# Optimization experiments

Measured on AMD Instinct MI355X. Metric: run time of the kernel, lower is better.

The kernel has to match this reference:

```python
import jax, jax.numpy as jnp
import numpy as np

B, T, C = 4, 2048, 1024
HEADS = 16
HEAD_DIM = C // HEADS
WINDOW = 256


def setup_inputs() -> dict:
    key = jax.random.key(0)
    k1, k2, k3 = jax.random.split(key, 3)
    x = jax.random.normal(k1, (B, T, C), dtype=jnp.float32)
    # torch nn.Linear weights: [out_features, in_features]; scale like kaiming-uniform-ish
    W_qkv = jax.random.normal(k2, (3 * C, C), dtype=jnp.float32) * (1.0 / np.sqrt(C))
    W_proj = jax.random.normal(k3, (C, C), dtype=jnp.float32) * (1.0 / np.sqrt(C))
    return {"x": x, "W_qkv": W_qkv, "W_proj": W_proj}


def reference(x, W_qkv, W_proj):
    b, t, c = x.shape
    h, d = HEADS, HEAD_DIM
    qkv = x @ W_qkv.T  # [b,t,3c]
    q, k, v = jnp.split(qkv, 3, axis=-1)
    q = q.reshape(b, t, h, d).transpose(0, 2, 1, 3)  # [b,h,t,d]
    k = k.reshape(b, t, h, d).transpose(0, 2, 1, 3)
    v = v.reshape(b, t, h, d).transpose(0, 2, 1, 3)
    scale = 1.0 / jnp.sqrt(jnp.asarray(d, dtype=q.dtype))
    scores = jnp.einsum('bhqd,bhkd->bhqk', q, k) * scale  # [b,h,t,t]
    i = jnp.arange(t)[:, None]
    j = jnp.arange(t)[None, :]
    mask = (j <= i) & (j > i - WINDOW)  # sliding-window causal band
    scores = jnp.where(mask, scores, -jnp.inf)
    attn = jax.nn.softmax(scores, axis=-1)
    y = jnp.einsum('bhqk,bhkd->bhqd', attn, v)  # [b,h,t,d]
    y = y.transpose(0, 2, 1, 3).reshape(b, t, c)
    return y @ W_proj.T
```

## Files before the change

### kernel.cpp

```cpp
#include <hip/hip_runtime.h>
#include <hip/hip_bf16.h>
#include <math.h>

#define BB 4
#define TT 2048
#define CC 1024
#define HH 16
#define DD 64
#define WW 256
#define MM (BB*TT)
#define NX (MM*CC)
#define NQ (3*CC*CC)
#define NP (CC*CC)

typedef __bf16 bf16x8 __attribute__((ext_vector_type(8)));
typedef __bf16 bf16x4 __attribute__((ext_vector_type(4)));
typedef float  f32x4  __attribute__((ext_vector_type(4)));

__device__ __forceinline__ void async_cp16(const void* g, void* l) {
  __builtin_amdgcn_global_load_lds(
      (const __attribute__((address_space(1))) void*)g,
      (__attribute__((address_space(3))) void*)l, 16, 0, 0);
}

__device__ __forceinline__ unsigned short f2bf(float v) {
  __hip_bfloat16 h = __float2bfloat16(v);
  return *(unsigned short*)&h;
}

__device__ __forceinline__ size_t wpk_off(int n, int k) {
  return ((((size_t)(n >> 7) * 16 + (k >> 6)) * 16) +
          (((k >> 3) & 7) * 2 + ((n >> 6) & 1))) * 512 +
         (size_t)(n & 63) * 8 + (k & 7);
}

__global__ __launch_bounds__(256)
void prep(const float* __restrict__ x,
          const float* __restrict__ wq,
          const float* __restrict__ wp,
          unsigned short* __restrict__ wpk,
          unsigned short* __restrict__ Apk) {
  const int p = blockIdx.x;
  const int tid = threadIdx.x;
  if (p < 4096) {
    int i = (p * 256 + tid) * 4;
    const float* src; unsigned short* dst; int n, k;
    if (i < NQ) { src = wq + i; n = i >> 10; k = i & 1023; dst = wpk; }
    else {
      int j = i - NQ;
      src = wp + j; n = j >> 10; k = j & 1023; dst = wpk + NQ;
    }
    float4 v = *(const float4*)src;
    size_t off = wpk_off(n, k);
    dst[off + 0] = f2bf(v.x);
    dst[off + 1] = f2bf(v.y);
    dst[off + 2] = f2bf(v.z);
    dst[off + 3] = f2bf(v.w);
    return;
  }
  __shared__ __align__(16) unsigned short tile[64 * 72];
  const int pid = p - 4096;
  const int bm = pid & 127;
  const int bk = pid >> 7;
  const int tr = tid >> 4;
  const int tc = (tid & 15) * 4;
#pragma unroll
  for (int i = 0; i < 4; i++) {
    int row = i * 16 + tr;
    float4 v = *(const float4*)&x[(size_t)(bm * 64 + row) * 1024 + bk * 64 + tc];
    tile[row * 72 + tc + 0] = f2bf(v.x);
    tile[row * 72 + tc + 1] = f2bf(v.y);
    tile[row * 72 + tc + 2] = f2bf(v.z);
    tile[row * 72 + tc + 3] = f2bf(v.w);
  }
  __syncthreads();
  const int w = tid >> 6, lane = tid & 63;
  const int quad = lane >> 4, l15 = lane & 15;
#pragma unroll
  for (int f = 0; f < 2; f++) {
    bf16x8 fr = *(const bf16x8*)&tile[(w * 16 + l15) * 72 + f * 32 + quad * 8];
    *(bf16x8*)&Apk[(((size_t)(bm * 4 + w) * 32) + bk * 2 + f) * 512 + lane * 8] = fr;
  }
}

__global__ __launch_bounds__(256, 2)
void gemm_qkv(const unsigned short* __restrict__ Apk,
              const unsigned short* __restrict__ Bw,
              unsigned short* __restrict__ Qh,
              unsigned short* __restrict__ Kh,
              unsigned short* __restrict__ Vt) {
  __shared__ __align__(16) unsigned short Bs[4][8192];

  const int id   = blockIdx.x;
  const int xcd  = id & 7;
  const int slot = id >> 3;
  const int mloc = slot / 24;
  const int nloc = slot % 24;
  const int m0 = (xcd * 4 + mloc) * 256;
  const int n0 = nloc * 128;

  const int tid  = threadIdx.x;
  const int w    = tid >> 6;
  const int lane = tid & 63;
  const int quad = lane >> 4;
  const int l15  = lane & 15;

  f32x4 acc[4][8];
#pragma unroll
  for (int i = 0; i < 4; i++)
#pragma unroll
    for (int j = 0; j < 8; j++) acc[i][j] = (f32x4)0.0f;

  const unsigned short* abase =
      Apk + ((size_t)((m0 >> 4) + w * 4) * 32) * 512 + lane * 8;

  const unsigned short* wb = Bw + (size_t)(n0 >> 7) * (16 * 16 * 512);

  auto stageB = [&](int kt, unsigned short* bs) {
#pragma unroll
    for (int i = 0; i < 4; i++) {
      int idx = w + 4 * i;
      async_cp16(wb + ((size_t)kt * 16 + idx) * 512 + lane * 8,
                 &bs[idx * 512]);
    }
  };

  bf16x8 Af[3][4];
  auto loadA = [&](int g, bf16x8* fr) {
#pragma unroll
    for (int tm = 0; tm < 4; tm++)
      fr[tm] = *(const bf16x8*)(abase + ((size_t)(tm * 32 + g)) * 512);
  };

  loadA(0, Af[0]);
  loadA(1, Af[1]);
  stageB(0, Bs[0]);
  stageB(1, Bs[1]);
  stageB(2, Bs[2]);
  asm volatile("s_waitcnt vmcnt(0)" ::: "memory");
  __builtin_amdgcn_sched_barrier(0);
  asm volatile("s_barrier" ::: "memory");

#pragma unroll
  for (int s = 0; s < 16; s++) {
    const unsigned short* bs = Bs[s & 3];
    if (s + 3 < 16) stageB(s + 3, Bs[(s + 3) & 3]);
#pragma unroll
    for (int sub = 0; sub < 2; sub++) {
      const int g = s * 2 + sub;
      if (g + 2 < 32) loadA(g + 2, Af[(g + 2) % 3]);
      const bf16x8* af = Af[g % 3];
      __builtin_amdgcn_s_setprio(1);
#pragma unroll
      for (int tn = 0; tn < 8; tn++) {
        bf16x8 bfv = *(const bf16x8*)
            &bs[(sub * 4 + quad) * 1024 + (tn * 16 + l15) * 8];
#pragma unroll
        for (int tm = 0; tm < 4; tm++)
          acc[tm][tn] = __builtin_amdgcn_mfma_f32_16x16x32_bf16(
              af[tm], bfv, acc[tm][tn], 0, 0, 0);
      }
      __builtin_amdgcn_s_setprio(0);
    }
    asm volatile("s_waitcnt vmcnt(16) lgkmcnt(0)" ::: "memory");
    __builtin_amdgcn_sched_barrier(0);
    asm volatile("s_barrier" ::: "memory");
  }

  const int t3 = n0 >> 10;
  if (t3 == 0) {
#pragma unroll
    for (int tm = 0; tm < 4; tm++)
#pragma unroll
      for (int tn = 0; tn < 8; tn++) {
        int colb = n0 + tn * 16;
        int hh = (colb >> 6) & 15;
        int dd = (colb & 63) + l15;
#pragma unroll
        for (int r = 0; r < 4; r++) {
          int row = m0 + w * 64 + tm * 16 + quad * 4 + r;
          int b = row >> 11, tt = row & 2047;
          Qh[((size_t)((b * 16 + hh) * 2048 + tt)) * 64 + dd] =
              f2bf(acc[tm][tn][r] * 0.125f);
        }
      }
  } else if (t3 == 1) {
#pragma unroll
    for (int tm = 0; tm < 4; tm++)
#pragma unroll
      for (int tn = 0; tn < 8; tn++) {
        int colb = n0 + tn * 16;
        int hh = (colb >> 6) & 15;
        int dd = (colb & 63) + l15;
#pragma unroll
        for (int r = 0; r < 4; r++) {
          int row = m0 + w * 64 + tm * 16 + quad * 4 + r;
          int b = row >> 11, tt = row & 2047;
          Kh[((((size_t)(b * 16 + hh) * 32 + (tt >> 6)) * 8 + (dd >> 3)) * 512)
             + (tt & 63) * 8 + (dd & 7)] = f2bf(acc[tm][tn][r]);
        }
      }
  } else {
    unsigned short* T = &Bs[0][0] + w * 4608;
    const int b    = (m0 + w * 64) >> 11;
    const int tc_g = ((m0 & 2047) >> 6) + w;
    const int h0   = (n0 >> 6) & 15;
#pragma unroll
    for (int hp = 0; hp < 2; hp++) {
#pragma unroll
      for (int tnl = 0; tnl < 4; tnl++)
#pragma unroll
        for (int tm = 0; tm < 4; tm++)
#pragma unroll
          for (int r = 0; r < 4; r++)
            T[(tnl * 16 + l15) * 72 + tm * 16 + quad * 4 + r] =
                f2bf(acc[tm][hp * 4 + tnl][r]);
      asm volatile("s_waitcnt lgkmcnt(0)" ::: "memory");
      const size_t base =
          ((size_t)((b * 16 + h0 + hp) * 32 + tc_g)) * 4096;
#pragma unroll
      for (int j = 0; j < 8; j++) {
        bf16x8 v = *(const bf16x8*)&T[lane * 72 + j * 8];
        *(bf16x8*)&Vt[base + (size_t)j * 512 + lane * 8] = v;
      }
    }
  }
}

__global__ __launch_bounds__(256, 2)
void gemm_proj(const unsigned short* __restrict__ Apk,
               const unsigned short* __restrict__ Bw,
               float* __restrict__ Co) {
  __shared__ __align__(16) unsigned short Bs[4][8192];

  const int id   = blockIdx.x;
  const int xcd  = id & 7;
  const int slot = id >> 3;
  const int mloc = slot >> 3;
  const int nloc = slot & 7;
  const int m0 = (xcd * 8 + mloc) * 128;
  const int n0 = nloc * 128;

  const int tid  = threadIdx.x;
  const int w    = tid >> 6;
  const int lane = tid & 63;
  const int quad = lane >> 4;
  const int l15  = lane & 15;

  f32x4 acc[2][8];
#pragma unroll
  for (int i = 0; i < 2; i++)
#pragma unroll
    for (int j = 0; j < 8; j++) acc[i][j] = (f32x4)0.0f;

  const unsigned short* abase =
      Apk + ((size_t)((m0 >> 4) + w * 2) * 32) * 512 + lane * 8;

  const unsigned short* wb = Bw + (size_t)(n0 >> 7) * (16 * 16 * 512);

  auto stageB = [&](int kt, unsigned short* bs) {
#pragma unroll
    for (int i = 0; i < 4; i++) {
      int idx = w + 4 * i;
      async_cp16(wb + ((size_t)kt * 16 + idx) * 512 + lane * 8,
                 &bs[idx * 512]);
    }
  };

  bf16x8 Af[3][2];
  auto loadA = [&](int g, bf16x8* fr) {
#pragma unroll
    for (int tm = 0; tm < 2; tm++)
      fr[tm] = *(const bf16x8*)(abase + ((size_t)(tm * 32 + g)) * 512);
  };

  loadA(0, Af[0]);
  loadA(1, Af[1]);
  stageB(0, Bs[0]);
  stageB(1, Bs[1]);
  stageB(2, Bs[2]);
  asm volatile("s_waitcnt vmcnt(0)" ::: "memory");
  __builtin_amdgcn_sched_barrier(0);
  asm volatile("s_barrier" ::: "memory");

#pragma unroll
  for (int s = 0; s < 16; s++) {
    const unsigned short* bs = Bs[s & 3];
    if (s + 3 < 16) stageB(s + 3, Bs[(s + 3) & 3]);
#pragma unroll
    for (int sub = 0; sub < 2; sub++) {
      const int g = s * 2 + sub;
      if (g + 2 < 32) loadA(g + 2, Af[(g + 2) % 3]);
      const bf16x8* af = Af[g % 3];
      __builtin_amdgcn_s_setprio(1);
#pragma unroll
      for (int tn = 0; tn < 8; tn++) {
        bf16x8 bfv = *(const bf16x8*)
            &bs[(sub * 4 + quad) * 1024 + (tn * 16 + l15) * 8];
#pragma unroll
        for (int tm = 0; tm < 2; tm++)
          acc[tm][tn] = __builtin_amdgcn_mfma_f32_16x16x32_bf16(
              af[tm], bfv, acc[tm][tn], 0, 0, 0);
      }
      __builtin_amdgcn_s_setprio(0);
    }
    if (s < 14)
      asm volatile("s_waitcnt vmcnt(12) lgkmcnt(0)" ::: "memory");
    else
      asm volatile("s_waitcnt vmcnt(8) lgkmcnt(0)" ::: "memory");
    __builtin_amdgcn_sched_barrier(0);
    asm volatile("s_barrier" ::: "memory");
  }

#pragma unroll
  for (int tm = 0; tm < 2; tm++)
#pragma unroll
    for (int tn = 0; tn < 8; tn++)
#pragma unroll
      for (int r = 0; r < 4; r++) {
        int row = m0 + w * 32 + tm * 16 + quad * 4 + r;
        int col = n0 + tn * 16 + l15;
        Co[(size_t)row * 1024 + col] = acc[tm][tn][r];
      }
}

__global__ __launch_bounds__(256, 2)
void attn_mfma(const unsigned short* __restrict__ Qh,
               const unsigned short* __restrict__ Kh,
               const unsigned short* __restrict__ Vt,
               unsigned short* __restrict__ Ypk) {
  __shared__ __align__(16) unsigned short SH[40960];

  const int tid  = threadIdx.x;
  const int w    = tid >> 6;
  const int lane = tid & 63;
  const int quad = lane >> 4;
  const int l15  = lane & 15;

  const int vid  = blockIdx.y * 32 + blockIdx.x;
  const int v    = (vid & 7) * 256 + (vid >> 3);
  const int bh   = v >> 5;
  const int q0   = (v & 31) << 6;

  const int c0 = (q0 >= 256) ? 0 : (4 - (q0 >> 6));

  const unsigned short* Qg = Qh + ((size_t)bh * 2048 + q0) * 64;
  bf16x8 Qf[2];
#pragma unroll
  for (int fs = 0; fs < 2; fs++)
    Qf[fs] = *(const bf16x8*)(Qg + (w * 16 + l15) * 64 + fs * 32 + quad * 8);

  const unsigned short* Kg = Kh + (size_t)bh * 32 * 4096;
  const unsigned short* Vg = Vt + (size_t)bh * 32 * 4096;
  for (int ch = c0; ch < 5; ch++) {
    int tc = (q0 >> 6) - 4 + ch;
#pragma unroll
    for (int i = 0; i < 2; i++) {
      int kc = w * 2 + i;
      async_cp16(Kg + ((size_t)tc * 8 + kc) * 512 + lane * 8,
                 &SH[ch * 4096 + kc * 512]);
    }
  }
  for (int ch = c0; ch < 5; ch++) {
    int tc = (q0 >> 6) - 4 + ch;
#pragma unroll
    for (int i = 0; i < 2; i++) {
      int kc = w * 2 + i;
      async_cp16(Vg + ((size_t)tc * 8 + kc) * 512 + lane * 8,
                 &SH[20480 + ch * 4096 + kc * 512]);
    }
  }
  if (c0 == 0)      asm volatile("s_waitcnt vmcnt(10)" ::: "memory");
  else if (c0 == 1) asm volatile("s_waitcnt vmcnt(8)"  ::: "memory");
  else if (c0 == 2) asm volatile("s_waitcnt vmcnt(6)"  ::: "memory");
  else if (c0 == 3) asm volatile("s_waitcnt vmcnt(4)"  ::: "memory");
  else              asm volatile("s_waitcnt vmcnt(2)"  ::: "memory");
  __builtin_amdgcn_sched_barrier(0);
  asm volatile("s_barrier" ::: "memory");

  f32x4 S[5][4];
#pragma unroll
  for (int ch = 0; ch < 5; ch++)
#pragma unroll
    for (int tn = 0; tn < 4; tn++) S[ch][tn] = (f32x4)0.0f;

#pragma unroll
  for (int ch = 0; ch < 5; ch++) {
    if (ch < c0) continue;
#pragma unroll
    for (int ks = 0; ks < 2; ks++) {
      int kc = ks * 4 + quad;
#pragma unroll
      for (int tn = 0; tn < 4; tn++) {
        bf16x8 bk = *(const bf16x8*)
            &SH[ch * 4096 + kc * 512 + (tn * 16 + l15) * 8];
        S[ch][tn] = __builtin_amdgcn_mfma_f32_16x16x32_bf16(
            Qf[ks], bk, S[ch][tn], 0, 0, 0);
      }
    }
  }

  const int qb = q0 + w * 16 + quad * 4;
  if (c0 == 0) {
#pragma unroll
    for (int tn = 0; tn < 4; tn++) {
      int j = q0 - 256 + tn * 16 + l15;
#pragma unroll
      for (int r = 0; r < 4; r++)
        if (qb + r > j + (WW - 1)) S[0][tn][r] = -__builtin_inff();
    }
  }
#pragma unroll
  for (int tn = 0; tn < 4; tn++) {
    int j = q0 + tn * 16 + l15;
#pragma unroll
    for (int r = 0; r < 4; r++)
      if (j > qb + r) S[4][tn][r] = -__builtin_inff();
  }

  float mrow[4], lrow[4];
#pragma unroll
  for (int r = 0; r < 4; r++) mrow[r] = -__builtin_inff();
#pragma unroll
  for (int ch = 0; ch < 5; ch++) {
    if (ch < c0) continue;
#pragma unroll
    for (int tn = 0; tn < 4; tn++)
#pragma unroll
      for (int r = 0; r < 4; r++)
        mrow[r] = fmaxf(mrow[r], S[ch][tn][r]);
  }
#pragma unroll
  for (int off = 1; off < 16; off <<= 1)
#pragma unroll
    for (int r = 0; r < 4; r++)
      mrow[r] = fmaxf(mrow[r], __shfl_xor(mrow[r], off));

#pragma unroll
  for (int r = 0; r < 4; r++) lrow[r] = 0.0f;
#pragma unroll
  for (int ch = 0; ch < 5; ch++) {
    if (ch < c0) continue;
#pragma unroll
    for (int tn = 0; tn < 4; tn++)
#pragma unroll
      for (int r = 0; r < 4; r++) {
        float e = __expf(S[ch][tn][r] - mrow[r]);
        S[ch][tn][r] = e;
        lrow[r] += e;
      }
  }
#pragma unroll
  for (int off = 1; off < 16; off <<= 1)
#pragma unroll
    for (int r = 0; r < 4; r++) lrow[r] += __shfl_xor(lrow[r], off);

  asm volatile("s_waitcnt vmcnt(0)" ::: "memory");
  __builtin_amdgcn_sched_barrier(0);
  asm volatile("s_barrier" ::: "memory");

  f32x4 Oacc[4];
#pragma unroll
  for (int td = 0; td < 4; td++) Oacc[td] = (f32x4)0.0f;

#pragma unroll
  for (int ch = 0; ch < 5; ch++) {
    if (ch < c0) continue;
    unsigned short* Ps = SH + (ch & 1) * 4608;
#pragma unroll
    for (int tn = 0; tn < 4; tn++)
#pragma unroll
      for (int r = 0; r < 4; r++)
        Ps[(w * 16 + quad * 4 + r) * 68 + tn * 16 + l15] = f2bf(S[ch][tn][r]);
    asm volatile("s_waitcnt lgkmcnt(0)" ::: "memory");
#pragma unroll
    for (int ks = 0; ks < 2; ks++) {
      int off = (w * 16 + l15) * 68 + ks * 32 + quad * 8;
      bf16x4 plo = *(const bf16x4*)&Ps[off];
      bf16x4 phi = *(const bf16x4*)&Ps[off + 4];
      bf16x8 ap = __builtin_shufflevector(plo, phi, 0, 1, 2, 3, 4, 5, 6, 7);
      int kc = ks * 4 + quad;
#pragma unroll
      for (int td = 0; td < 4; td++) {
        bf16x8 bv = *(const bf16x8*)
            &SH[20480 + ch * 4096 + kc * 512 + (td * 16 + l15) * 8];
        Oacc[td] = __builtin_amdgcn_mfma_f32_16x16x32_bf16(
            ap, bv, Oacc[td], 0, 0, 0);
      }
    }
  }

  const int b = bh >> 4, h = bh & 15;
  float inv[4];
#pragma unroll
  for (int r = 0; r < 4; r++) inv[r] = 1.0f / lrow[r];
  unsigned short* Ot = SH + 10240;
#pragma unroll
  for (int td = 0; td < 4; td++)
#pragma unroll
    for (int r = 0; r < 4; r++)
      Ot[(w * 16 + quad * 4 + r) * 72 + td * 16 + l15] =
          f2bf(Oacc[td][r] * inv[r]);
  asm volatile("s_waitcnt lgkmcnt(0)" ::: "memory");
  const size_t rt = (size_t)((b * 2048 + q0) >> 4) + w;
#pragma unroll
  for (int f = 0; f < 2; f++) {
    bf16x8 fr = *(const bf16x8*)&Ot[(w * 16 + l15) * 72 + f * 32 + quad * 8];
    *(bf16x8*)&Ypk[(rt * 32 + h * 2 + f) * 512 + lane * 8] = fr;
  }
}

extern "C" void kernel_launch(void* const* d_in, const int* in_sizes, int n_in,
                              void* d_out, int out_size, void* d_ws, size_t ws_size,
                              hipStream_t stream) {
  const float* x     = (const float*)d_in[0];
  const float* wqkv  = (const float*)d_in[1];
  const float* wproj = (const float*)d_in[2];
  float* out = (float*)d_out;

  char* ws = (char*)d_ws;
  unsigned short* apk    = (unsigned short*)(ws);
  unsigned short* wqkvb  = (unsigned short*)(ws + (size_t)16 * 1024 * 1024);
  unsigned short* wprojb = (unsigned short*)(ws + (size_t)22 * 1024 * 1024);
  unsigned short* qh     = (unsigned short*)(ws + (size_t)24 * 1024 * 1024);
  unsigned short* kh     = (unsigned short*)(ws + (size_t)40 * 1024 * 1024);
  unsigned short* vt     = (unsigned short*)(ws + (size_t)56 * 1024 * 1024);
  unsigned short* ypk    = (unsigned short*)(ws + (size_t)72 * 1024 * 1024);

  prep<<<4096 + 2048, 256, 0, stream>>>(x, wqkv, wproj, wqkvb, apk);

  gemm_qkv<<<768, 256, 0, stream>>>(apk, wqkvb, qh, kh, vt);

  attn_mfma<<<dim3(TT / 64, BB * HH), 256, 0, stream>>>(
      qh, kh, vt, ypk);

  gemm_proj<<<512, 256, 0, stream>>>(ypk, wprojb, out);
}
```

Before: 202.7 us.

## Split GEMM k-steps into four phases interleaving LDS reads, async copies and MFMAs

Both the QKV and projection GEMM main loops now split each k-stage into four phases. Each phase reads four B fragments from LDS, issues one async global-to-LDS copy and the A prefetch, then runs a block of MFMAs between two barriers. The prologue issues the B stages before the A loads and waits only on partial vmcnt instead of draining everything. The goal is to spread memory traffic evenly through the MFMA work and overlap it better, at the cost of more barriers per stage and vmcnt counts that are fragile to get right.

New measurement: 200.4 us. Within noise of the previous version (-1.1%).

```diff
diff --git a/kernel.cpp b/kernel.cpp
--- a/kernel.cpp
+++ b/kernel.cpp
@@ -132,39 +132,54 @@
       fr[tm] = *(const bf16x8*)(abase + ((size_t)(tm * 32 + g)) * 512);
   };
 
-  loadA(0, Af[0]);
-  loadA(1, Af[1]);
   stageB(0, Bs[0]);
   stageB(1, Bs[1]);
   stageB(2, Bs[2]);
-  asm volatile("s_waitcnt vmcnt(0)" ::: "memory");
+  loadA(0, Af[0]);
+  loadA(1, Af[1]);
+  asm volatile("s_waitcnt vmcnt(16)" ::: "memory");
   __builtin_amdgcn_sched_barrier(0);
-  asm volatile("s_barrier" ::: "memory");
+  __builtin_amdgcn_s_barrier();
 
 #pragma unroll
   for (int s = 0; s < 16; s++) {
     const unsigned short* bs = Bs[s & 3];
-    if (s + 3 < 16) stageB(s + 3, Bs[(s + 3) & 3]);
-#pragma unroll
-    for (int sub = 0; sub < 2; sub++) {
-      const int g = s * 2 + sub;
-      if (g + 2 < 32) loadA(g + 2, Af[(g + 2) % 3]);
+    unsigned short* bn = Bs[(s + 3) & 3];
+#pragma unroll
+    for (int ph = 0; ph < 4; ph++) {
+      const int ksub = ph >> 1;
+      const int th   = ph & 1;
+      const int g    = s * 2 + ksub;
+      bf16x8 bfv[4];
+#pragma unroll
+      for (int j = 0; j < 4; j++)
+        bfv[j] = *(const bf16x8*)
+            &bs[(ksub * 4 + quad) * 1024 + ((th * 4 + j) * 16 + l15) * 8];
+      if (s + 3 < 16)
+        async_cp16(wb + ((size_t)(s + 3) * 16 + (w + 4 * ph)) * 512 + lane * 8,
+                   &bn[(w + 4 * ph) * 512]);
+      if ((ph & 1) == 0 && g + 2 < 32) loadA(g + 2, Af[(g + 2) % 3]);
+      __builtin_amdgcn_s_barrier();
+      asm volatile("s_waitcnt lgkmcnt(0)" ::: "memory");
+      __builtin_amdgcn_sched_barrier(0);
       const bf16x8* af = Af[g % 3];
       __builtin_amdgcn_s_setprio(1);
 #pragma unroll
-      for (int tn = 0; tn < 8; tn++) {
-        bf16x8 bfv = *(const bf16x8*)
-            &bs[(sub * 4 + quad) * 1024 + (tn * 16 + l15) * 8];
+      for (int j = 0; j < 4; j++)
 #pragma unroll
         for (int tm = 0; tm < 4; tm++)
-          acc[tm][tn] = __builtin_amdgcn_mfma_f32_16x16x32_bf16(
-              af[tm], bfv, acc[tm][tn], 0, 0, 0);
-      }
+          acc[tm][th * 4 + j] = __builtin_amdgcn_mfma_f32_16x16x32_bf16(
+              af[tm], bfv[j], acc[tm][th * 4 + j], 0, 0, 0);
       __builtin_amdgcn_s_setprio(0);
-    }
-    asm volatile("s_waitcnt vmcnt(16) lgkmcnt(0)" ::: "memory");
-    __builtin_amdgcn_sched_barrier(0);
-    asm volatile("s_barrier" ::: "memory");
+      __builtin_amdgcn_sched_barrier(0);
+      if (ph == 3 && s < 15) {
+        if (s <= 12)      asm volatile("s_waitcnt vmcnt(24)" ::: "memory");
+        else if (s == 13) asm volatile("s_waitcnt vmcnt(20)" ::: "memory");
+        else              asm volatile("s_waitcnt vmcnt(16)" ::: "memory");
+        __builtin_amdgcn_sched_barrier(0);
+      }
+      __builtin_amdgcn_s_barrier();
+    }
   }
 
   const int t3 = n0 >> 10;
@@ -274,42 +289,54 @@
       fr[tm] = *(const bf16x8*)(abase + ((size_t)(tm * 32 + g)) * 512);
   };
 
-  loadA(0, Af[0]);
-  loadA(1, Af[1]);
   stageB(0, Bs[0]);
   stageB(1, Bs[1]);
   stageB(2, Bs[2]);
-  asm volatile("s_waitcnt vmcnt(0)" ::: "memory");
+  loadA(0, Af[0]);
+  loadA(1, Af[1]);
+  asm volatile("s_waitcnt vmcnt(12)" ::: "memory");
   __builtin_amdgcn_sched_barrier(0);
-  asm volatile("s_barrier" ::: "memory");
+  __builtin_amdgcn_s_barrier();
 
 #pragma unroll
   for (int s = 0; s < 16; s++) {
     const unsigned short* bs = Bs[s & 3];
-    if (s + 3 < 16) stageB(s + 3, Bs[(s + 3) & 3]);
-#pragma unroll
-    for (int sub = 0; sub < 2; sub++) {
-      const int g = s * 2 + sub;
-      if (g + 2 < 32) loadA(g + 2, Af[(g + 2) % 3]);
+    unsigned short* bn = Bs[(s + 3) & 3];
+#pragma unroll
+    for (int ph = 0; ph < 4; ph++) {
+      const int ksub = ph >> 1;
+      const int th   = ph & 1;
+      const int g    = s * 2 + ksub;
+      bf16x8 bfv[4];
+#pragma unroll
+      for (int j = 0; j < 4; j++)
+        bfv[j] = *(const bf16x8*)
+            &bs[(ksub * 4 + quad) * 1024 + ((th * 4 + j) * 16 + l15) * 8];
+      if (s + 3 < 16)
+        async_cp16(wb + ((size_t)(s + 3) * 16 + (w + 4 * ph)) * 512 + lane * 8,
+                   &bn[(w + 4 * ph) * 512]);
+      if ((ph & 1) == 0 && g + 2 < 32) loadA(g + 2, Af[(g + 2) % 3]);
+      __builtin_amdgcn_s_barrier();
+      asm volatile("s_waitcnt lgkmcnt(0)" ::: "memory");
+      __builtin_amdgcn_sched_barrier(0);
       const bf16x8* af = Af[g % 3];
       __builtin_amdgcn_s_setprio(1);
 #pragma unroll
-      for (int tn = 0; tn < 8; tn++) {
-        bf16x8 bfv = *(const bf16x8*)
-            &bs[(sub * 4 + quad) * 1024 + (tn * 16 + l15) * 8];
+      for (int j = 0; j < 4; j++)
 #pragma unroll
         for (int tm = 0; tm < 2; tm++)
-          acc[tm][tn] = __builtin_amdgcn_mfma_f32_16x16x32_bf16(
-              af[tm], bfv, acc[tm][tn], 0, 0, 0);
-      }
+          acc[tm][th * 4 + j] = __builtin_amdgcn_mfma_f32_16x16x32_bf16(
+              af[tm], bfv[j], acc[tm][th * 4 + j], 0, 0, 0);
       __builtin_amdgcn_s_setprio(0);
-    }
-    if (s < 14)
-      asm volatile("s_waitcnt vmcnt(12) lgkmcnt(0)" ::: "memory");
-    else
-      asm volatile("s_waitcnt vmcnt(8) lgkmcnt(0)" ::: "memory");
-    __builtin_amdgcn_sched_barrier(0);
-    asm volatile("s_barrier" ::: "memory");
+      __builtin_amdgcn_sched_barrier(0);
+      if (ph == 3 && s < 15) {
+        if (s <= 12)      asm volatile("s_waitcnt vmcnt(16)" ::: "memory");
+        else if (s == 13) asm volatile("s_waitcnt vmcnt(12)" ::: "memory");
+        else              asm volatile("s_waitcnt vmcnt(8)"  ::: "memory");
+        __builtin_amdgcn_sched_barrier(0);
+      }
+      __builtin_amdgcn_s_barrier();
+    }
   }
 
 #pragma unroll
```
